# Optimization experiments

Measured on AMD Instinct MI355X. Metric: run time of the kernel, lower is better.

Reference implementation:

```python
import jax, jax.numpy as jnp
import numpy as np

D_MODEL = 1024
HIDDEN = 2048
D_STATE = 16
KERN = 3
BATCH = 2
SEQ = 2048


def _layernorm(x, g, b, eps=1e-5):
    m = jnp.mean(x, axis=-1, keepdims=True)
    v = jnp.var(x, axis=-1, keepdims=True)
    return (x - m) * jax.lax.rsqrt(v + eps) * g + b


def setup_inputs() -> dict:
    key = jax.random.key(0)
    ks = jax.random.split(key, 10)
    w_scale = 0.02  # keep pre-activations in a sane range (mimics trained-net init)
    return {
        "x": jax.random.normal(ks[0], (BATCH, SEQ, D_MODEL), jnp.float32),
        "W_x": jax.random.normal(ks[1], (HIDDEN, D_MODEL), jnp.float32) * w_scale,
        "b_x": jnp.zeros((HIDDEN,), jnp.float32),
        "W_g": jax.random.normal(ks[2], (HIDDEN, D_MODEL), jnp.float32) * w_scale,
        "b_g": jnp.zeros((HIDDEN,), jnp.float32),
        "conv_w": jax.random.normal(ks[3], (HIDDEN, 1, KERN), jnp.float32) * 0.3,
        "conv_b": jnp.zeros((HIDDEN,), jnp.float32),
        "A_raw": jax.random.normal(ks[4], (HIDDEN, D_STATE), jnp.float32),
        "B_ssm": jax.random.normal(ks[5], (HIDDEN, D_STATE), jnp.float32),
        "C_ssm": jax.random.normal(ks[6], (HIDDEN, D_STATE), jnp.float32),
        "W_dt": jax.random.normal(ks[7], (HIDDEN, D_MODEL), jnp.float32) * w_scale,
        "b_dt": jnp.zeros((HIDDEN,), jnp.float32),
        "W_out": jax.random.normal(ks[8], (D_MODEL, HIDDEN), jnp.float32) * w_scale,
        "b_out": jnp.zeros((D_MODEL,), jnp.float32),
        "ln_g": jnp.ones((D_MODEL,), jnp.float32),
        "ln_b": jnp.zeros((D_MODEL,), jnp.float32),
    }


def reference(x, W_x, b_x, W_g, b_g, conv_w, conv_b, A_raw, B_ssm, C_ssm,
              W_dt, b_dt, W_out, b_out, ln_g, ln_b):
    # projections: u, gate
    u = jnp.einsum('bld,hd->blh', x, W_x) + b_x                    # [B,L,H]
    g = jax.nn.sigmoid(jnp.einsum('bld,hd->blh', x, W_g) + b_g)    # [B,L,H]
    # depthwise conv over time (padding = kernel//2, 'same' for odd kernel)
    pad = conv_w.shape[-1] // 2
    h = jax.lax.conv_general_dilated(
        jnp.transpose(u, (0, 2, 1)), conv_w,
        window_strides=(1,), padding=[(pad, pad)],
        feature_group_count=conv_w.shape[0],
        dimension_numbers=('NCH', 'OIH', 'NCH')) + conv_b[None, :, None]
    h = jnp.transpose(h, (0, 2, 1))                                # [B,L,H]
    u = u * g + h * (1.0 - g)
    # time-invariant dt per channel (mean over batch & time, clamped)
    dt = jax.nn.softplus(jnp.einsum('bld,hd->blh', x, W_dt) + b_dt).mean(axis=(0, 1))
    dt = jnp.clip(dt, 1e-3, 2.0)                                   # [H]
    # discretize
    A = -jax.nn.softplus(A_raw)                                    # [H,S]
    A_d = jnp.exp(A * dt[:, None])                                 # [H,S]
    B_d = (A_d - 1.0) / (A + 1e-6) * B_ssm                         # [H,S]
    # selective scan: state s[b,h,k] = A_d*s + B_d*u_t ; y = <s, C>
    Bsz, L, H = u.shape
    S = A_d.shape[1]

    def step(carry, u_t):                                          # u_t: [B,H]
        new = A_d[None] * carry + B_d[None] * u_t[:, :, None]      # [B,H,S]
        y_t = jnp.einsum('bhs,hs->bh', new, C_ssm)
        return new, y_t

    init = jnp.zeros((Bsz, H, S), dtype=u.dtype)
    _, ys = jax.lax.scan(step, init, jnp.transpose(u, (1, 0, 2)))  # ys: [L,B,H]
    y = jnp.transpose(ys, (1, 0, 2))                               # [B,L,H]
    out = jnp.einsum('blh,dh->bld', y, W_out) + b_out
    return _layernorm(x + out, ln_g, ln_b)
```

## Files before the change

### kernel.cpp

```cpp
#include <hip/hip_runtime.h>
#include <math.h>

#define D_MODEL 1024
#define HIDDEN  2048
#define D_STATE 16
#define BATCH   2
#define SEQ     2048
#define NTOK    (BATCH*SEQ)
#define CHUNK   64
#define NCHUNK  (SEQ/CHUNK)

typedef __attribute__((ext_vector_type(8))) short bf16x8;
typedef __attribute__((ext_vector_type(8))) unsigned short ushort8;
typedef __attribute__((ext_vector_type(4))) float f32x4;

#define GLOAD_LDS16(gptr, lptr) \
    __builtin_amdgcn_global_load_lds((const __attribute__((address_space(1))) void*)(gptr), \
                                     (__attribute__((address_space(3))) void*)(lptr), 16, 0, 0)

__device__ __forceinline__ float softplus_f(float x) {
    return fmaxf(x, 0.0f) + log1pf(expf(-fabsf(x)));
}
__device__ __forceinline__ float sigmoid_f(float x) {
    return 1.0f / (1.0f + expf(-x));
}
__device__ __forceinline__ ushort f2bf(float f) {
    unsigned u = __float_as_uint(f);
    unsigned r = (u + 0x7fffu + ((u >> 16) & 1u)) >> 16;
    return (ushort)r;
}
__device__ __forceinline__ float bf2f(ushort u) {
    return __uint_as_float(((unsigned)u) << 16);
}

__global__ __launch_bounds__(256) void cvt_all(
    const float* __restrict__ x, const float* __restrict__ Wx,
    const float* __restrict__ Wg, const float* __restrict__ Wdt,
    const float* __restrict__ Wout, ushort* __restrict__ arena)
{
    int i = blockIdx.x * 256 + threadIdx.x;
    const float* src; int base;
    if      (i < 1048576) { src = x;    base = 0; }
    else if (i < 1572864) { src = Wx;   base = 1048576; }
    else if (i < 2097152) { src = Wg;   base = 1572864; }
    else if (i < 2621440) { src = Wdt;  base = 2097152; }
    else                  { src = Wout; base = 2621440; }
    float4 v = reinterpret_cast<const float4*>(src)[i - base];
    ushort4 o = { f2bf(v.x), f2bf(v.y), f2bf(v.z), f2bf(v.w) };
    reinterpret_cast<ushort4*>(arena)[i] = o;
}

__device__ __forceinline__ void kloop_dbuf(
    const ushort* __restrict__ A, const ushort* __restrict__ B,
    int K, int m0, int n0, ushort* As, ushort* Bs,
    f32x4 (&acc)[4][4], int lane, int w, int wm, int wn)
{
    const int lr   = lane >> 2;
    const int kc   = (lane & 3) * 8;
    const int quad = lane >> 4;
    const int fr   = lane & 15;

    const int slab0 = w * 2;
    const int r0 = slab0 * 16 + lr;
    const int r1 = r0 + 16;
    const size_t ga0 = (size_t)(m0 + r0) * K + kc;
    const size_t ga1 = (size_t)(m0 + r1) * K + kc;
    const size_t gb0 = (size_t)(n0 + r0) * K + kc;
    const size_t gb1 = (size_t)(n0 + r1) * K + kc;

    GLOAD_LDS16(A + ga0, &As[slab0 * 512]);
    GLOAD_LDS16(A + ga1, &As[slab0 * 512 + 512]);
    GLOAD_LDS16(B + gb0, &Bs[slab0 * 512]);
    GLOAD_LDS16(B + gb1, &Bs[slab0 * 512 + 512]);

    int buf = 0;
    for (int k0 = 0; k0 < K; k0 += 32) {
        __syncthreads();
        if (k0 + 32 < K) {
            const int nb = (buf ^ 1) * 4096;
            GLOAD_LDS16(A + ga0 + k0 + 32, &As[nb + slab0 * 512]);
            GLOAD_LDS16(A + ga1 + k0 + 32, &As[nb + slab0 * 512 + 512]);
            GLOAD_LDS16(B + gb0 + k0 + 32, &Bs[nb + slab0 * 512]);
            GLOAD_LDS16(B + gb1 + k0 + 32, &Bs[nb + slab0 * 512 + 512]);
        }
        const ushort* as = &As[buf * 4096];
        const ushort* bs = &Bs[buf * 4096];
        bf16x8 af[4], bfv[4];
        #pragma unroll
        for (int t = 0; t < 4; t++) {
            af[t]  = *reinterpret_cast<const bf16x8*>(&as[(wm * 64 + t * 16 + fr) * 32 + quad * 8]);
            bfv[t] = *reinterpret_cast<const bf16x8*>(&bs[(wn * 64 + t * 16 + fr) * 32 + quad * 8]);
        }
        #pragma unroll
        for (int i = 0; i < 4; i++)
            #pragma unroll
            for (int j = 0; j < 4; j++)
                acc[i][j] = __builtin_amdgcn_mfma_f32_16x16x32_bf16(af[i], bfv[j], acc[i][j], 0, 0, 0);
        buf ^= 1;
    }
}

__global__ __launch_bounds__(256) void proj_gemm_fused(
    const ushort* __restrict__ xbf, const ushort* __restrict__ Wcat,
    const float* __restrict__ b_x, const float* __restrict__ b_g,
    const float* __restrict__ b_dt, ushort* __restrict__ u_out,
    ushort* __restrict__ g_out, float* __restrict__ dt_sum)
{
    __shared__ ushort S[16384];
    ushort* As = S;
    ushort* Bs = S + 8192;
    const int tid = threadIdx.x, lane = tid & 63, w = tid >> 6;
    const int wm = w & 1, wn = w >> 1;
    const int m0 = blockIdx.y * 128, n0 = blockIdx.x * 128;
    const int quad = lane >> 4, fr = lane & 15;

    f32x4 acc[4][4];
    #pragma unroll
    for (int i = 0; i < 4; i++)
        #pragma unroll
        for (int j = 0; j < 4; j++)
            acc[i][j] = (f32x4){0.f, 0.f, 0.f, 0.f};

    kloop_dbuf(xbf, Wcat, D_MODEL, m0, n0, As, Bs, acc, lane, w, wm, wn);

    const int region = n0 >> 11;
    const int ncb = n0 & 2047;

    if (region == 2) {
        #pragma unroll
        for (int j = 0; j < 4; j++) {
            int n = ncb + wn * 64 + j * 16 + fr;
            float bj = b_dt[n];
            float s = 0.f;
            #pragma unroll
            for (int i = 0; i < 4; i++)
                #pragma unroll
                for (int r = 0; r < 4; r++)
                    s += softplus_f(acc[i][j][r] + bj);
            s += __shfl_xor(s, 16);
            s += __shfl_xor(s, 32);
            if (lane < 16) atomicAdd(&dt_sum[n], s);
        }
    } else {
        const float* bias = region ? b_g : b_x;
        ushort* out = region ? g_out : u_out;
        __syncthreads();
        ushort* Cs = S;
        #pragma unroll
        for (int j = 0; j < 4; j++) {
            int col = wn * 64 + j * 16 + fr;
            float bj = bias[ncb + col];
            #pragma unroll
            for (int i = 0; i < 4; i++) {
                int row = wm * 64 + i * 16 + quad * 4;
                #pragma unroll
                for (int r = 0; r < 4; r++) {
                    float v = acc[i][j][r] + bj;
                    if (region) v = sigmoid_f(v);
                    Cs[(row + r) * 128 + col] = f2bf(v);
                }
            }
        }
        __syncthreads();
        #pragma unroll
        for (int k = 0; k < 8; k++) {
            int v = k * 256 + tid;
            int row = v >> 4, c = (v & 15) * 8;
            *reinterpret_cast<ushort8*>(&out[(size_t)(m0 + row) * HIDDEN + ncb + c]) =
                *reinterpret_cast<const ushort8*>(&Cs[v * 8]);
        }
    }
}

__global__ __launch_bounds__(256) void gemm_out(
    const ushort* __restrict__ ybf, const ushort* __restrict__ Wout,
    const float* __restrict__ b_out, const float* __restrict__ x,
    float* __restrict__ resid)
{
    __shared__ ushort S[16384];
    ushort* As = S;
    ushort* Bs = S + 8192;
    const int tid = threadIdx.x, lane = tid & 63, w = tid >> 6;
    const int wm = w & 1, wn = w >> 1;
    const int m0 = blockIdx.y * 128, n0 = blockIdx.x * 128;
    const int quad = lane >> 4, fr = lane & 15;

    f32x4 acc[4][4];
    #pragma unroll
    for (int i = 0; i < 4; i++)
        #pragma unroll
        for (int j = 0; j < 4; j++)
            acc[i][j] = (f32x4){0.f, 0.f, 0.f, 0.f};

    kloop_dbuf(ybf, Wout, HIDDEN, m0, n0, As, Bs, acc, lane, w, wm, wn);

    float* Sf = (float*)S;
    __syncthreads();
    #pragma unroll
    for (int phase = 0; phase < 2; phase++) {
        if (wm == phase) {
            #pragma unroll
            for (int j = 0; j < 4; j++) {
                int col = wn * 64 + j * 16 + fr;
                float bj = b_out[n0 + col];
                #pragma unroll
                for (int i = 0; i < 4; i++) {
                    int row = i * 16 + quad * 4;
                    #pragma unroll
                    for (int r = 0; r < 4; r++)
                        Sf[(row + r) * 128 + col] = acc[i][j][r] + bj;
                }
            }
        }
        __syncthreads();
        #pragma unroll
        for (int k = 0; k < 8; k++) {
            int v = k * 256 + tid;
            int row = v >> 5, c = (v & 31) * 4;
            size_t off = (size_t)(m0 + phase * 64 + row) * D_MODEL + n0 + c;
            float4 xa = *reinterpret_cast<const float4*>(&x[off]);
            float4 cv = *reinterpret_cast<const float4*>(&Sf[v * 4]);
            float4 o = { cv.x + xa.x, cv.y + xa.y, cv.z + xa.z, cv.w + xa.w };
            *reinterpret_cast<float4*>(&resid[off]) = o;
        }
        __syncthreads();
    }
}

__global__ __launch_bounds__(256) void dt_finalize(
    const float* __restrict__ dt_sum, const float* __restrict__ A_raw,
    const float* __restrict__ B_ssm, float* __restrict__ A_d,
    float* __restrict__ B_d, float* __restrict__ A_dL)
{
    int i = blockIdx.x * 256 + threadIdx.x;
    if (i >= HIDDEN * D_STATE) return;
    int h = i >> 4;
    float dt = dt_sum[h] * (1.0f / NTOK);
    dt = fminf(fmaxf(dt, 1e-3f), 2.0f);
    float Av = -softplus_f(A_raw[i]);
    float Ad = expf(Av * dt);
    float Bd = (Ad - 1.0f) / (Av + 1e-6f) * B_ssm[i];
    A_d[i] = Ad;
    B_d[i] = Bd;
    A_dL[i] = expf(Av * dt * CHUNK);
}

__global__ __launch_bounds__(256) void scan_pass1(
    const ushort* __restrict__ u_bf, const ushort* __restrict__ g_bf,
    const float* __restrict__ conv_w, const float* __restrict__ conv_b,
    const float* __restrict__ A_d, const float* __restrict__ B_d,
    const float* __restrict__ C_ssm,
    ushort* __restrict__ ypart, float* __restrict__ states)
{
    int idx = blockIdx.x * 256 + threadIdx.x;
    int h  = idx & (HIDDEN - 1);
    int bc = idx >> 11;
    int c  = bc & (NCHUNK - 1);
    int b  = bc >> 5;
    float Ad[D_STATE], Bd[D_STATE], Cv[D_STATE], st[D_STATE];
    const float4* a4 = reinterpret_cast<const float4*>(A_d  + h * D_STATE);
    const float4* b4 = reinterpret_cast<const float4*>(B_d  + h * D_STATE);
    const float4* c4 = reinterpret_cast<const float4*>(C_ssm + h * D_STATE);
    #pragma unroll
    for (int q = 0; q < 4; q++) {
        float4 av = a4[q], bv = b4[q], cv = c4[q];
        Ad[q*4+0]=av.x; Ad[q*4+1]=av.y; Ad[q*4+2]=av.z; Ad[q*4+3]=av.w;
        Bd[q*4+0]=bv.x; Bd[q*4+1]=bv.y; Bd[q*4+2]=bv.z; Bd[q*4+3]=bv.w;
        Cv[q*4+0]=cv.x; Cv[q*4+1]=cv.y; Cv[q*4+2]=cv.z; Cv[q*4+3]=cv.w;
    }
    #pragma unroll
    for (int s = 0; s < D_STATE; s++) st[s] = 0.f;

    float w0 = conv_w[h * 3 + 0], w1 = conv_w[h * 3 + 1];
    float w2 = conv_w[h * 3 + 2], cb = conv_b[h];
    const int tok0 = c * CHUNK;
    const size_t base = ((size_t)b * SEQ + tok0) * HIDDEN + h;
    float u_prev = (tok0 > 0) ? bf2f(u_bf[base - HIDDEN]) : 0.f;
    float u_cur  = bf2f(u_bf[base]);
    for (int l = 0; l < CHUNK; l++) {
        float u_next = (tok0 + l + 1 < SEQ) ? bf2f(u_bf[base + (size_t)(l + 1) * HIDDEN]) : 0.f;
        float gv = bf2f(g_bf[base + (size_t)l * HIDDEN]);
        float conv = u_prev * w0 + u_cur * w1 + u_next * w2 + cb;
        float uv = u_cur * gv + conv * (1.0f - gv);
        float yv = 0.f;
        #pragma unroll
        for (int s = 0; s < D_STATE; s++) {
            st[s] = fmaf(Ad[s], st[s], Bd[s] * uv);
            yv = fmaf(st[s], Cv[s], yv);
        }
        ypart[base + (size_t)l * HIDDEN] = f2bf(yv);
        u_prev = u_cur; u_cur = u_next;
    }
    float4* sp = reinterpret_cast<float4*>(states + ((size_t)bc * HIDDEN + h) * D_STATE);
    #pragma unroll
    for (int q = 0; q < 4; q++)
        sp[q] = (float4){st[q*4+0], st[q*4+1], st[q*4+2], st[q*4+3]};
}

__global__ __launch_bounds__(256) void scan_pass2(
    float* __restrict__ states, const float* __restrict__ A_dL)
{
    int idx = blockIdx.x * 256 + threadIdx.x;
    int s = idx & 15;
    int h = (idx >> 4) & (HIDDEN - 1);
    int b = idx >> 15;
    float aL = A_dL[h * D_STATE + s];
    float carry = 0.f;
    for (int c = 0; c < NCHUNK; c++) {
        size_t addr = (((size_t)(b * NCHUNK + c) * HIDDEN) + h) * D_STATE + s;
        float fin = states[addr];
        states[addr] = carry;
        carry = fmaf(aL, carry, fin);
    }
}

__global__ __launch_bounds__(256) void scan_pass3(
    const ushort* __restrict__ ypart, const float* __restrict__ states,
    const float* __restrict__ A_d, const float* __restrict__ C_ssm,
    ushort* __restrict__ ybf)
{
    int idx = blockIdx.x * 256 + threadIdx.x;
    int h  = idx & (HIDDEN - 1);
    int bc = idx >> 11;
    int c  = bc & (NCHUNK - 1);
    int b  = bc >> 5;
    float Ad[D_STATE], t[D_STATE];
    const float* sp = states + ((size_t)bc * HIDDEN + h) * D_STATE;
    #pragma unroll
    for (int s = 0; s < D_STATE; s++) {
        float a = A_d[h * D_STATE + s];
        Ad[s] = a;
        t[s] = C_ssm[h * D_STATE + s] * a * sp[s];
    }
    const size_t base = ((size_t)b * SEQ + (size_t)c * CHUNK) * HIDDEN + h;
    for (int l = 0; l < CHUNK; l++) {
        float corr = 0.f;
        #pragma unroll
        for (int s = 0; s < D_STATE; s++) {
            corr += t[s];
            t[s] *= Ad[s];
        }
        ybf[base + (size_t)l * HIDDEN] = f2bf(bf2f(ypart[base + (size_t)l * HIDDEN]) + corr);
    }
}

__global__ __launch_bounds__(256) void ln_kernel(
    const float* __restrict__ resid, const float* __restrict__ ln_g,
    const float* __restrict__ ln_b, float* __restrict__ out)
{
    int row = blockIdx.x;
    int tid = threadIdx.x;
    const float4 v = reinterpret_cast<const float4*>(resid + (size_t)row * D_MODEL)[tid];
    float s  = v.x + v.y + v.z + v.w;
    float ss = v.x * v.x + v.y * v.y + v.z * v.z + v.w * v.w;
    #pragma unroll
    for (int off = 32; off > 0; off >>= 1) {
        s  += __shfl_down(s, off);
        ss += __shfl_down(ss, off);
    }
    __shared__ float sbuf[4], ssbuf[4];
    int wid = tid >> 6, lane = tid & 63;
    if (lane == 0) { sbuf[wid] = s; ssbuf[wid] = ss; }
    __syncthreads();
    float tot  = sbuf[0] + sbuf[1] + sbuf[2] + sbuf[3];
    float tot2 = ssbuf[0] + ssbuf[1] + ssbuf[2] + ssbuf[3];
    float mean = tot * (1.0f / D_MODEL);
    float var  = tot2 * (1.0f / D_MODEL) - mean * mean;
    float rstd = rsqrtf(var + 1e-5f);
    const float4 gv = reinterpret_cast<const float4*>(ln_g)[tid];
    const float4 bv = reinterpret_cast<const float4*>(ln_b)[tid];
    float4 o;
    o.x = (v.x - mean) * rstd * gv.x + bv.x;
    o.y = (v.y - mean) * rstd * gv.y + bv.y;
    o.z = (v.z - mean) * rstd * gv.z + bv.z;
    o.w = (v.w - mean) * rstd * gv.w + bv.w;
    reinterpret_cast<float4*>(out + (size_t)row * D_MODEL)[tid] = o;
}

extern "C" void kernel_launch(void* const* d_in, const int* in_sizes, int n_in,
                              void* d_out, int out_size, void* d_ws, size_t ws_size,
                              hipStream_t stream) {
    const float* x      = (const float*)d_in[0];
    const float* W_x    = (const float*)d_in[1];
    const float* b_x    = (const float*)d_in[2];
    const float* W_g    = (const float*)d_in[3];
    const float* b_g    = (const float*)d_in[4];
    const float* conv_w = (const float*)d_in[5];
    const float* conv_b = (const float*)d_in[6];
    const float* A_raw  = (const float*)d_in[7];
    const float* B_ssm  = (const float*)d_in[8];
    const float* C_ssm  = (const float*)d_in[9];
    const float* W_dt   = (const float*)d_in[10];
    const float* b_dt   = (const float*)d_in[11];
    const float* W_out  = (const float*)d_in[12];
    const float* b_out  = (const float*)d_in[13];
    const float* ln_g   = (const float*)d_in[14];
    const float* ln_b   = (const float*)d_in[15];

    char* W = (char*)d_ws;
    ushort* arena   = (ushort*)(W);
    ushort* x_bf    = arena;
    ushort* Wcat    = arena + 4194304;
    ushort* Wout_bf = arena + 10485760;
    ushort* u_bf    = (ushort*)(W + (24ull << 20));
    ushort* g_bf    = (ushort*)(W + (40ull << 20));
    ushort* ypart   = (ushort*)(W + (56ull << 20));
    float*  resid   = (float*)(W + (40ull << 20));
    float*  states  = (float*)(W + (72ull << 20));
    float*  dt_sum  = (float*)(W + (80ull << 20));
    float*  A_d     = (float*)(W + (80ull << 20) + 65536);
    float*  B_d     = (float*)(W + (80ull << 20) + 65536 + 131072);
    float*  A_dL    = (float*)(W + (80ull << 20) + 65536 + 262144);
    ushort* y_bf    = u_bf;

    hipMemsetAsync(dt_sum, 0, HIDDEN * sizeof(float), stream);

    dim3 blk(256);
    cvt_all<<<12288, blk, 0, stream>>>(x, W_x, W_g, W_dt, W_out, arena);

    dim3 grid_proj(3 * HIDDEN / 128, NTOK / 128);
    proj_gemm_fused<<<grid_proj, blk, 0, stream>>>(x_bf, Wcat, b_x, b_g, b_dt,
                                                   u_bf, g_bf, dt_sum);
    dt_finalize<<<(HIDDEN * D_STATE) / 256, blk, 0, stream>>>(dt_sum, A_raw, B_ssm,
                                                              A_d, B_d, A_dL);
    scan_pass1<<<(BATCH * NCHUNK * HIDDEN) / 256, blk, 0, stream>>>(
        u_bf, g_bf, conv_w, conv_b, A_d, B_d, C_ssm, ypart, states);
    scan_pass2<<<(BATCH * HIDDEN * D_STATE) / 256, blk, 0, stream>>>(states, A_dL);
    scan_pass3<<<(BATCH * NCHUNK * HIDDEN) / 256, blk, 0, stream>>>(ypart, states, A_d,
                                                                    C_ssm, y_bf);
    dim3 grid_out(D_MODEL / 128, NTOK / 128);
    gemm_out<<<grid_out, blk, 0, stream>>>(y_bf, Wout_bf, b_out, x, resid);
    ln_kernel<<<NTOK, blk, 0, stream>>>(resid, ln_g, ln_b, (float*)d_out);
}
```

Measured before the change: 318.0 us.

## Fold dt discretization into scan kernels, retile output GEMM, swap grid order

Removes the dt_finalize kernel and its A_d/B_d/A_dL buffers; the scan passes now recompute the discretized A and B from dt_sum and A_raw inline. The output GEMM becomes 64x128 tiles on 128-thread blocks with its own inlined double-buffered k-loop, doubling the block count to give more parallelism. Both GEMM grids are transposed so that consecutive blocks walk along M, which changes weight reuse in L2. Scan inner loops split the reduction across several accumulators to shorten dependency chains, at the cost of redundant exp/softplus work per thread.

```diff
diff --git a/kernel.cpp b/kernel.cpp
--- a/kernel.cpp
+++ b/kernel.cpp
@@ -111,7 +111,7 @@
     ushort* Bs = S + 8192;
     const int tid = threadIdx.x, lane = tid & 63, w = tid >> 6;
     const int wm = w & 1, wn = w >> 1;
-    const int m0 = blockIdx.y * 128, n0 = blockIdx.x * 128;
+    const int m0 = blockIdx.x * 128, n0 = blockIdx.y * 128;
     const int quad = lane >> 4, fr = lane & 15;
 
     f32x4 acc[4][4];
@@ -172,18 +172,20 @@
     }
 }
 
-__global__ __launch_bounds__(256) void gemm_out(
+__global__ __launch_bounds__(128) void gemm_out(
     const ushort* __restrict__ ybf, const ushort* __restrict__ Wout,
     const float* __restrict__ b_out, const float* __restrict__ x,
     float* __restrict__ resid)
 {
     __shared__ ushort S[16384];
     ushort* As = S;
-    ushort* Bs = S + 8192;
+    ushort* Bs = S + 4096;
     const int tid = threadIdx.x, lane = tid & 63, w = tid >> 6;
-    const int wm = w & 1, wn = w >> 1;
-    const int m0 = blockIdx.y * 128, n0 = blockIdx.x * 128;
+    const int wn = w;
+    const int m0 = blockIdx.x * 64, n0 = blockIdx.y * 128;
     const int quad = lane >> 4, fr = lane & 15;
+    const int lr = lane >> 2, kc = (lane & 3) * 8;
+    const int K = HIDDEN;
 
     f32x4 acc[4][4];
     #pragma unroll
@@ -192,64 +194,79 @@
         for (int j = 0; j < 4; j++)
             acc[i][j] = (f32x4){0.f, 0.f, 0.f, 0.f};
 
-    kloop_dbuf(ybf, Wout, HIDDEN, m0, n0, As, Bs, acc, lane, w, wm, wn);
+    const int sa0 = w * 2, sa1 = w * 2 + 1;
+    size_t gaddrA0 = (size_t)(m0 + sa0 * 16 + lr) * K + kc;
+    size_t gaddrA1 = (size_t)(m0 + sa1 * 16 + lr) * K + kc;
+    size_t gaddrB[4];
+    #pragma unroll
+    for (int j = 0; j < 4; j++)
+        gaddrB[j] = (size_t)(n0 + (w * 4 + j) * 16 + lr) * K + kc;
+
+    GLOAD_LDS16(ybf + gaddrA0, &As[sa0 * 512]);
+    GLOAD_LDS16(ybf + gaddrA1, &As[sa1 * 512]);
+    #pragma unroll
+    for (int j = 0; j < 4; j++)
+        GLOAD_LDS16(Wout + gaddrB[j], &Bs[(w * 4 + j) * 512]);
+
+    int buf = 0;
+    for (int k0 = 0; k0 < K; k0 += 32) {
+        __syncthreads();
+        if (k0 + 32 < K) {
+            const int nbA = (buf ^ 1) * 2048, nbB = (buf ^ 1) * 4096;
+            GLOAD_LDS16(ybf + gaddrA0 + k0 + 32, &As[nbA + sa0 * 512]);
+            GLOAD_LDS16(ybf + gaddrA1 + k0 + 32, &As[nbA + sa1 * 512]);
+            #pragma unroll
+            for (int j = 0; j < 4; j++)
+                GLOAD_LDS16(Wout + gaddrB[j] + k0 + 32, &Bs[nbB + (w * 4 + j) * 512]);
+        }
+        const ushort* as = &As[buf * 2048];
+        const ushort* bs = &Bs[buf * 4096];
+        bf16x8 af[4], bfv[4];
+        #pragma unroll
+        for (int t = 0; t < 4; t++) {
+            af[t]  = *reinterpret_cast<const bf16x8*>(&as[(t * 16 + fr) * 32 + quad * 8]);
+            bfv[t] = *reinterpret_cast<const bf16x8*>(&bs[(wn * 64 + t * 16 + fr) * 32 + quad * 8]);
+        }
+        #pragma unroll
+        for (int i = 0; i < 4; i++)
+            #pragma unroll
+            for (int j = 0; j < 4; j++)
+                acc[i][j] = __builtin_amdgcn_mfma_f32_16x16x32_bf16(af[i], bfv[j], acc[i][j], 0, 0, 0);
+        buf ^= 1;
+    }
 
     float* Sf = (float*)S;
     __syncthreads();
     #pragma unroll
-    for (int phase = 0; phase < 2; phase++) {
-        if (wm == phase) {
-            #pragma unroll
-            for (int j = 0; j < 4; j++) {
-                int col = wn * 64 + j * 16 + fr;
-                float bj = b_out[n0 + col];
-                #pragma unroll
-                for (int i = 0; i < 4; i++) {
-                    int row = i * 16 + quad * 4;
-                    #pragma unroll
-                    for (int r = 0; r < 4; r++)
-                        Sf[(row + r) * 128 + col] = acc[i][j][r] + bj;
-                }
-            }
-        }
-        __syncthreads();
-        #pragma unroll
-        for (int k = 0; k < 8; k++) {
-            int v = k * 256 + tid;
-            int row = v >> 5, c = (v & 31) * 4;
-            size_t off = (size_t)(m0 + phase * 64 + row) * D_MODEL + n0 + c;
-            float4 xa = *reinterpret_cast<const float4*>(&x[off]);
-            float4 cv = *reinterpret_cast<const float4*>(&Sf[v * 4]);
-            float4 o = { cv.x + xa.x, cv.y + xa.y, cv.z + xa.z, cv.w + xa.w };
-            *reinterpret_cast<float4*>(&resid[off]) = o;
-        }
-        __syncthreads();
-    }
-}
-
-__global__ __launch_bounds__(256) void dt_finalize(
-    const float* __restrict__ dt_sum, const float* __restrict__ A_raw,
-    const float* __restrict__ B_ssm, float* __restrict__ A_d,
-    float* __restrict__ B_d, float* __restrict__ A_dL)
-{
-    int i = blockIdx.x * 256 + threadIdx.x;
-    if (i >= HIDDEN * D_STATE) return;
-    int h = i >> 4;
-    float dt = dt_sum[h] * (1.0f / NTOK);
-    dt = fminf(fmaxf(dt, 1e-3f), 2.0f);
-    float Av = -softplus_f(A_raw[i]);
-    float Ad = expf(Av * dt);
-    float Bd = (Ad - 1.0f) / (Av + 1e-6f) * B_ssm[i];
-    A_d[i] = Ad;
-    B_d[i] = Bd;
-    A_dL[i] = expf(Av * dt * CHUNK);
+    for (int j = 0; j < 4; j++) {
+        int col = wn * 64 + j * 16 + fr;
+        float bj = b_out[n0 + col];
+        #pragma unroll
+        for (int i = 0; i < 4; i++) {
+            int row = i * 16 + quad * 4;
+            #pragma unroll
+            for (int r = 0; r < 4; r++)
+                Sf[(row + r) * 128 + col] = acc[i][j][r] + bj;
+        }
+    }
+    __syncthreads();
+    #pragma unroll
+    for (int k = 0; k < 16; k++) {
+        int v = k * 128 + tid;
+        int row = v >> 5, c = (v & 31) * 4;
+        size_t off = (size_t)(m0 + row) * D_MODEL + n0 + c;
+        float4 xa = *reinterpret_cast<const float4*>(&x[off]);
+        float4 cv = *reinterpret_cast<const float4*>(&Sf[v * 4]);
+        float4 o = { cv.x + xa.x, cv.y + xa.y, cv.z + xa.z, cv.w + xa.w };
+        *reinterpret_cast<float4*>(&resid[off]) = o;
+    }
 }
 
 __global__ __launch_bounds__(256) void scan_pass1(
     const ushort* __restrict__ u_bf, const ushort* __restrict__ g_bf,
     const float* __restrict__ conv_w, const float* __restrict__ conv_b,
-    const float* __restrict__ A_d, const float* __restrict__ B_d,
-    const float* __restrict__ C_ssm,
+    const float* __restrict__ dt_sum, const float* __restrict__ A_raw,
+    const float* __restrict__ B_ssm, const float* __restrict__ C_ssm,
     ushort* __restrict__ ypart, float* __restrict__ states)
 {
     int idx = blockIdx.x * 256 + threadIdx.x;
@@ -257,19 +274,17 @@
     int bc = idx >> 11;
     int c  = bc & (NCHUNK - 1);
     int b  = bc >> 5;
+    float dt = fminf(fmaxf(dt_sum[h] * (1.0f / NTOK), 1e-3f), 2.0f);
     float Ad[D_STATE], Bd[D_STATE], Cv[D_STATE], st[D_STATE];
-    const float4* a4 = reinterpret_cast<const float4*>(A_d  + h * D_STATE);
-    const float4* b4 = reinterpret_cast<const float4*>(B_d  + h * D_STATE);
-    const float4* c4 = reinterpret_cast<const float4*>(C_ssm + h * D_STATE);
-    #pragma unroll
-    for (int q = 0; q < 4; q++) {
-        float4 av = a4[q], bv = b4[q], cv = c4[q];
-        Ad[q*4+0]=av.x; Ad[q*4+1]=av.y; Ad[q*4+2]=av.z; Ad[q*4+3]=av.w;
-        Bd[q*4+0]=bv.x; Bd[q*4+1]=bv.y; Bd[q*4+2]=bv.z; Bd[q*4+3]=bv.w;
-        Cv[q*4+0]=cv.x; Cv[q*4+1]=cv.y; Cv[q*4+2]=cv.z; Cv[q*4+3]=cv.w;
-    }
-    #pragma unroll
-    for (int s = 0; s < D_STATE; s++) st[s] = 0.f;
+    #pragma unroll
+    for (int s = 0; s < D_STATE; s++) {
+        float Av = -softplus_f(A_raw[h * D_STATE + s]);
+        float a = expf(Av * dt);
+        Ad[s] = a;
+        Bd[s] = (a - 1.0f) / (Av + 1e-6f) * B_ssm[h * D_STATE + s];
+        Cv[s] = C_ssm[h * D_STATE + s];
+        st[s] = 0.f;
+    }
 
     float w0 = conv_w[h * 3 + 0], w1 = conv_w[h * 3 + 1];
     float w2 = conv_w[h * 3 + 2], cb = conv_b[h];
@@ -282,13 +297,19 @@
         float gv = bf2f(g_bf[base + (size_t)l * HIDDEN]);
         float conv = u_prev * w0 + u_cur * w1 + u_next * w2 + cb;
         float uv = u_cur * gv + conv * (1.0f - gv);
-        float yv = 0.f;
-        #pragma unroll
-        for (int s = 0; s < D_STATE; s++) {
-            st[s] = fmaf(Ad[s], st[s], Bd[s] * uv);
-            yv = fmaf(st[s], Cv[s], yv);
-        }
-        ypart[base + (size_t)l * HIDDEN] = f2bf(yv);
+        float y0 = 0.f, y1 = 0.f, y2 = 0.f, y3 = 0.f;
+        #pragma unroll
+        for (int s = 0; s < D_STATE; s += 4) {
+            st[s+0] = fmaf(Ad[s+0], st[s+0], Bd[s+0] * uv);
+            st[s+1] = fmaf(Ad[s+1], st[s+1], Bd[s+1] * uv);
+            st[s+2] = fmaf(Ad[s+2], st[s+2], Bd[s+2] * uv);
+            st[s+3] = fmaf(Ad[s+3], st[s+3], Bd[s+3] * uv);
+            y0 = fmaf(st[s+0], Cv[s+0], y0);
+            y1 = fmaf(st[s+1], Cv[s+1], y1);
+            y2 = fmaf(st[s+2], Cv[s+2], y2);
+            y3 = fmaf(st[s+3], Cv[s+3], y3);
+        }
+        ypart[base + (size_t)l * HIDDEN] = f2bf((y0 + y1) + (y2 + y3));
         u_prev = u_cur; u_cur = u_next;
     }
     float4* sp = reinterpret_cast<float4*>(states + ((size_t)bc * HIDDEN + h) * D_STATE);
@@ -298,13 +319,16 @@
 }
 
 __global__ __launch_bounds__(256) void scan_pass2(
-    float* __restrict__ states, const float* __restrict__ A_dL)
+    float* __restrict__ states, const float* __restrict__ dt_sum,
+    const float* __restrict__ A_raw)
 {
     int idx = blockIdx.x * 256 + threadIdx.x;
     int s = idx & 15;
     int h = (idx >> 4) & (HIDDEN - 1);
     int b = idx >> 15;
-    float aL = A_dL[h * D_STATE + s];
+    float dt = fminf(fmaxf(dt_sum[h] * (1.0f / NTOK), 1e-3f), 2.0f);
+    float Av = -softplus_f(A_raw[h * D_STATE + s]);
+    float aL = expf(Av * dt * CHUNK);
     float carry = 0.f;
     for (int c = 0; c < NCHUNK; c++) {
         size_t addr = (((size_t)(b * NCHUNK + c) * HIDDEN) + h) * D_STATE + s;
@@ -316,31 +340,35 @@
 
 __global__ __launch_bounds__(256) void scan_pass3(
     const ushort* __restrict__ ypart, const float* __restrict__ states,
-    const float* __restrict__ A_d, const float* __restrict__ C_ssm,
-    ushort* __restrict__ ybf)
+    const float* __restrict__ dt_sum, const float* __restrict__ A_raw,
+    const float* __restrict__ C_ssm, ushort* __restrict__ ybf)
 {
     int idx = blockIdx.x * 256 + threadIdx.x;
     int h  = idx & (HIDDEN - 1);
     int bc = idx >> 11;
     int c  = bc & (NCHUNK - 1);
     int b  = bc >> 5;
+    float dt = fminf(fmaxf(dt_sum[h] * (1.0f / NTOK), 1e-3f), 2.0f);
     float Ad[D_STATE], t[D_STATE];
     const float* sp = states + ((size_t)bc * HIDDEN + h) * D_STATE;
     #pragma unroll
     for (int s = 0; s < D_STATE; s++) {
-        float a = A_d[h * D_STATE + s];
+        float Av = -softplus_f(A_raw[h * D_STATE + s]);
+        float a = expf(Av * dt);
         Ad[s] = a;
         t[s] = C_ssm[h * D_STATE + s] * a * sp[s];
     }
     const size_t base = ((size_t)b * SEQ + (size_t)c * CHUNK) * HIDDEN + h;
     for (int l = 0; l < CHUNK; l++) {
-        float corr = 0.f;
-        #pragma unroll
-        for (int s = 0; s < D_STATE; s++) {
-            corr += t[s];
+        float c0 = 0.f, c1 = 0.f;
+        #pragma unroll
+        for (int s = 0; s < D_STATE; s += 2) {
+            c0 += t[s];
+            c1 += t[s + 1];
             t[s] *= Ad[s];
-        }
-        ybf[base + (size_t)l * HIDDEN] = f2bf(bf2f(ypart[base + (size_t)l * HIDDEN]) + corr);
+            t[s + 1] *= Ad[s + 1];
+        }
+        ybf[base + (size_t)l * HIDDEN] = f2bf(bf2f(ypart[base + (size_t)l * HIDDEN]) + (c0 + c1));
     }
 }
 
@@ -408,9 +436,6 @@
     float*  resid   = (float*)(W + (40ull << 20));
     float*  states  = (float*)(W + (72ull << 20));
     float*  dt_sum  = (float*)(W + (80ull << 20));
-    float*  A_d     = (float*)(W + (80ull << 20) + 65536);
-    float*  B_d     = (float*)(W + (80ull << 20) + 65536 + 131072);
-    float*  A_dL    = (float*)(W + (80ull << 20) + 65536 + 262144);
     ushort* y_bf    = u_bf;
 
     hipMemsetAsync(dt_sum, 0, HIDDEN * sizeof(float), stream);
@@ -418,17 +443,15 @@
     dim3 blk(256);
     cvt_all<<<12288, blk, 0, stream>>>(x, W_x, W_g, W_dt, W_out, arena);
 
-    dim3 grid_proj(3 * HIDDEN / 128, NTOK / 128);
+    dim3 grid_proj(NTOK / 128, 3 * HIDDEN / 128);
     proj_gemm_fused<<<grid_proj, blk, 0, stream>>>(x_bf, Wcat, b_x, b_g, b_dt,
                                                    u_bf, g_bf, dt_sum);
-    dt_finalize<<<(HIDDEN * D_STATE) / 256, blk, 0, stream>>>(dt_sum, A_raw, B_ssm,
-                                                              A_d, B_d, A_dL);
     scan_pass1<<<(BATCH * NCHUNK * HIDDEN) / 256, blk, 0, stream>>>(
-        u_bf, g_bf, conv_w, conv_b, A_d, B_d, C_ssm, ypart, states);
-    scan_pass2<<<(BATCH * HIDDEN * D_STATE) / 256, blk, 0, stream>>>(states, A_dL);
-    scan_pass3<<<(BATCH * NCHUNK * HIDDEN) / 256, blk, 0, stream>>>(ypart, states, A_d,
-                                                                    C_ssm, y_bf);
-    dim3 grid_out(D_MODEL / 128, NTOK / 128);
-    gemm_out<<<grid_out, blk, 0, stream>>>(y_bf, Wout_bf, b_out, x, resid);
+        u_bf, g_bf, conv_w, conv_b, dt_sum, A_raw, B_ssm, C_ssm, ypart, states);
+    scan_pass2<<<(BATCH * HIDDEN * D_STATE) / 256, blk, 0, stream>>>(states, dt_sum, A_raw);
+    scan_pass3<<<(BATCH * NCHUNK * HIDDEN) / 256, blk, 0, stream>>>(ypart, states, dt_sum,
+                                                                    A_raw, C_ssm, y_bf);
+    dim3 grid_out(NTOK / 64, D_MODEL / 128);
+    gemm_out<<<grid_out, dim3(128), 0, stream>>>(y_bf, Wout_bf, b_out, x, resid);
     ln_kernel<<<NTOK, blk, 0, stream>>>(resid, ln_g, ln_b, (float*)d_out);
 }
```

After: 323.2 us. Within noise of the previous version (+1.6%).

## Triple-buffer GEMM k-loop with explicit waitcnt, swap grid order, split scan FMA chains

Applied to the files above, without the earlier changes.

Replaces the double-buffered LDS k-loop in both GEMMs with a three-stage pipeline. Loads are issued two iterations ahead and synchronised with explicit s_waitcnt vmcnt(4) and s_barrier, which hides more global latency at the cost of extra LDS. The launch grid is transposed so consecutive blocks walk the M dimension, which changes L2 reuse of the weight tiles. The scan pass1 and pass3 reductions are split into several independent accumulators to shorten dependent FMA and add chains.

```diff
diff --git a/kernel.cpp b/kernel.cpp
--- a/kernel.cpp
+++ b/kernel.cpp
@@ -50,7 +50,7 @@
     reinterpret_cast<ushort4*>(arena)[i] = o;
 }
 
-__device__ __forceinline__ void kloop_dbuf(
+__device__ __forceinline__ void kloop_pipe3(
     const ushort* __restrict__ A, const ushort* __restrict__ B,
     int K, int m0, int n0, ushort* As, ushort* Bs,
     f32x4 (&acc)[4][4], int lane, int w, int wm, int wn)
@@ -68,21 +68,27 @@
     const size_t gb0 = (size_t)(n0 + r0) * K + kc;
     const size_t gb1 = (size_t)(n0 + r1) * K + kc;
 
-    GLOAD_LDS16(A + ga0, &As[slab0 * 512]);
-    GLOAD_LDS16(A + ga1, &As[slab0 * 512 + 512]);
-    GLOAD_LDS16(B + gb0, &Bs[slab0 * 512]);
-    GLOAD_LDS16(B + gb1, &Bs[slab0 * 512 + 512]);
+    const int niter = K / 32;
+    GLOAD_LDS16(A + ga0,      &As[slab0 * 512]);
+    GLOAD_LDS16(A + ga1,      &As[slab0 * 512 + 512]);
+    GLOAD_LDS16(B + gb0,      &Bs[slab0 * 512]);
+    GLOAD_LDS16(B + gb1,      &Bs[slab0 * 512 + 512]);
+    GLOAD_LDS16(A + ga0 + 32, &As[4096 + slab0 * 512]);
+    GLOAD_LDS16(A + ga1 + 32, &As[4096 + slab0 * 512 + 512]);
+    GLOAD_LDS16(B + gb0 + 32, &Bs[4096 + slab0 * 512]);
+    GLOAD_LDS16(B + gb1 + 32, &Bs[4096 + slab0 * 512 + 512]);
 
     int buf = 0;
-    for (int k0 = 0; k0 < K; k0 += 32) {
-        __syncthreads();
-        if (k0 + 32 < K) {
-            const int nb = (buf ^ 1) * 4096;
-            GLOAD_LDS16(A + ga0 + k0 + 32, &As[nb + slab0 * 512]);
-            GLOAD_LDS16(A + ga1 + k0 + 32, &As[nb + slab0 * 512 + 512]);
-            GLOAD_LDS16(B + gb0 + k0 + 32, &Bs[nb + slab0 * 512]);
-            GLOAD_LDS16(B + gb1 + k0 + 32, &Bs[nb + slab0 * 512 + 512]);
-        }
+    for (int i = 0; i < niter; i++) {
+        asm volatile("s_waitcnt vmcnt(4) lgkmcnt(0)" ::: "memory");
+        asm volatile("s_barrier" ::: "memory");
+        int nb = buf + 2; if (nb >= 3) nb -= 3;
+        const size_t koff = (i + 2 < niter) ? (size_t)(i + 2) * 32 : 0;
+        GLOAD_LDS16(A + ga0 + koff, &As[nb * 4096 + slab0 * 512]);
+        GLOAD_LDS16(A + ga1 + koff, &As[nb * 4096 + slab0 * 512 + 512]);
+        GLOAD_LDS16(B + gb0 + koff, &Bs[nb * 4096 + slab0 * 512]);
+        GLOAD_LDS16(B + gb1 + koff, &Bs[nb * 4096 + slab0 * 512 + 512]);
+
         const ushort* as = &As[buf * 4096];
         const ushort* bs = &Bs[buf * 4096];
         bf16x8 af[4], bfv[4];
@@ -92,12 +98,14 @@
             bfv[t] = *reinterpret_cast<const bf16x8*>(&bs[(wn * 64 + t * 16 + fr) * 32 + quad * 8]);
         }
         #pragma unroll
-        for (int i = 0; i < 4; i++)
+        for (int ii = 0; ii < 4; ii++)
             #pragma unroll
-            for (int j = 0; j < 4; j++)
-                acc[i][j] = __builtin_amdgcn_mfma_f32_16x16x32_bf16(af[i], bfv[j], acc[i][j], 0, 0, 0);
-        buf ^= 1;
-    }
+            for (int jj = 0; jj < 4; jj++)
+                acc[ii][jj] = __builtin_amdgcn_mfma_f32_16x16x32_bf16(af[ii], bfv[jj], acc[ii][jj], 0, 0, 0);
+        buf = (buf == 2) ? 0 : buf + 1;
+    }
+    asm volatile("s_waitcnt vmcnt(0) lgkmcnt(0)" ::: "memory");
+    asm volatile("s_barrier" ::: "memory");
 }
 
 __global__ __launch_bounds__(256) void proj_gemm_fused(
@@ -106,12 +114,12 @@
     const float* __restrict__ b_dt, ushort* __restrict__ u_out,
     ushort* __restrict__ g_out, float* __restrict__ dt_sum)
 {
-    __shared__ ushort S[16384];
+    __shared__ ushort S[24576];
     ushort* As = S;
-    ushort* Bs = S + 8192;
+    ushort* Bs = S + 12288;
     const int tid = threadIdx.x, lane = tid & 63, w = tid >> 6;
     const int wm = w & 1, wn = w >> 1;
-    const int m0 = blockIdx.y * 128, n0 = blockIdx.x * 128;
+    const int m0 = blockIdx.x * 128, n0 = blockIdx.y * 128;
     const int quad = lane >> 4, fr = lane & 15;
 
     f32x4 acc[4][4];
@@ -121,7 +129,7 @@
         for (int j = 0; j < 4; j++)
             acc[i][j] = (f32x4){0.f, 0.f, 0.f, 0.f};
 
-    kloop_dbuf(xbf, Wcat, D_MODEL, m0, n0, As, Bs, acc, lane, w, wm, wn);
+    kloop_pipe3(xbf, Wcat, D_MODEL, m0, n0, As, Bs, acc, lane, w, wm, wn);
 
     const int region = n0 >> 11;
     const int ncb = n0 & 2047;
@@ -144,7 +152,6 @@
     } else {
         const float* bias = region ? b_g : b_x;
         ushort* out = region ? g_out : u_out;
-        __syncthreads();
         ushort* Cs = S;
         #pragma unroll
         for (int j = 0; j < 4; j++) {
@@ -177,12 +184,12 @@
     const float* __restrict__ b_out, const float* __restrict__ x,
     float* __restrict__ resid)
 {
-    __shared__ ushort S[16384];
+    __shared__ ushort S[24576];
     ushort* As = S;
-    ushort* Bs = S + 8192;
+    ushort* Bs = S + 12288;
     const int tid = threadIdx.x, lane = tid & 63, w = tid >> 6;
     const int wm = w & 1, wn = w >> 1;
-    const int m0 = blockIdx.y * 128, n0 = blockIdx.x * 128;
+    const int m0 = blockIdx.x * 128, n0 = blockIdx.y * 128;
     const int quad = lane >> 4, fr = lane & 15;
 
     f32x4 acc[4][4];
@@ -192,10 +199,9 @@
         for (int j = 0; j < 4; j++)
             acc[i][j] = (f32x4){0.f, 0.f, 0.f, 0.f};
 
-    kloop_dbuf(ybf, Wout, HIDDEN, m0, n0, As, Bs, acc, lane, w, wm, wn);
+    kloop_pipe3(ybf, Wout, HIDDEN, m0, n0, As, Bs, acc, lane, w, wm, wn);
 
     float* Sf = (float*)S;
-    __syncthreads();
     #pragma unroll
     for (int phase = 0; phase < 2; phase++) {
         if (wm == phase) {
@@ -282,13 +288,19 @@
         float gv = bf2f(g_bf[base + (size_t)l * HIDDEN]);
         float conv = u_prev * w0 + u_cur * w1 + u_next * w2 + cb;
         float uv = u_cur * gv + conv * (1.0f - gv);
-        float yv = 0.f;
-        #pragma unroll
-        for (int s = 0; s < D_STATE; s++) {
-            st[s] = fmaf(Ad[s], st[s], Bd[s] * uv);
-            yv = fmaf(st[s], Cv[s], yv);
-        }
-        ypart[base + (size_t)l * HIDDEN] = f2bf(yv);
+        float y0 = 0.f, y1 = 0.f, y2 = 0.f, y3 = 0.f;
+        #pragma unroll
+        for (int s = 0; s < D_STATE; s += 4) {
+            st[s+0] = fmaf(Ad[s+0], st[s+0], Bd[s+0] * uv);
+            st[s+1] = fmaf(Ad[s+1], st[s+1], Bd[s+1] * uv);
+            st[s+2] = fmaf(Ad[s+2], st[s+2], Bd[s+2] * uv);
+            st[s+3] = fmaf(Ad[s+3], st[s+3], Bd[s+3] * uv);
+            y0 = fmaf(st[s+0], Cv[s+0], y0);
+            y1 = fmaf(st[s+1], Cv[s+1], y1);
+            y2 = fmaf(st[s+2], Cv[s+2], y2);
+            y3 = fmaf(st[s+3], Cv[s+3], y3);
+        }
+        ypart[base + (size_t)l * HIDDEN] = f2bf((y0 + y1) + (y2 + y3));
         u_prev = u_cur; u_cur = u_next;
     }
     float4* sp = reinterpret_cast<float4*>(states + ((size_t)bc * HIDDEN + h) * D_STATE);
@@ -334,13 +346,15 @@
     }
     const size_t base = ((size_t)b * SEQ + (size_t)c * CHUNK) * HIDDEN + h;
     for (int l = 0; l < CHUNK; l++) {
-        float corr = 0.f;
-        #pragma unroll
-        for (int s = 0; s < D_STATE; s++) {
-            corr += t[s];
+        float c0 = 0.f, c1 = 0.f;
+        #pragma unroll
+        for (int s = 0; s < D_STATE; s += 2) {
+            c0 += t[s];
+            c1 += t[s + 1];
             t[s] *= Ad[s];
-        }
-        ybf[base + (size_t)l * HIDDEN] = f2bf(bf2f(ypart[base + (size_t)l * HIDDEN]) + corr);
+            t[s + 1] *= Ad[s + 1];
+        }
+        ybf[base + (size_t)l * HIDDEN] = f2bf(bf2f(ypart[base + (size_t)l * HIDDEN]) + (c0 + c1));
     }
 }
 
@@ -418,7 +432,7 @@
     dim3 blk(256);
     cvt_all<<<12288, blk, 0, stream>>>(x, W_x, W_g, W_dt, W_out, arena);
 
-    dim3 grid_proj(3 * HIDDEN / 128, NTOK / 128);
+    dim3 grid_proj(NTOK / 128, 3 * HIDDEN / 128);
     proj_gemm_fused<<<grid_proj, blk, 0, stream>>>(x_bf, Wcat, b_x, b_g, b_dt,
                                                    u_bf, g_bf, dt_sum);
     dt_finalize<<<(HIDDEN * D_STATE) / 256, blk, 0, stream>>>(dt_sum, A_raw, B_ssm,
@@ -428,7 +442,7 @@
     scan_pass2<<<(BATCH * HIDDEN * D_STATE) / 256, blk, 0, stream>>>(states, A_dL);
     scan_pass3<<<(BATCH * NCHUNK * HIDDEN) / 256, blk, 0, stream>>>(ypart, states, A_d,
                                                                     C_ssm, y_bf);
-    dim3 grid_out(D_MODEL / 128, NTOK / 128);
+    dim3 grid_out(NTOK / 128, D_MODEL / 128);
     gemm_out<<<grid_out, blk, 0, stream>>>(y_bf, Wout_bf, b_out, x, resid);
     ln_kernel<<<NTOK, blk, 0, stream>>>(resid, ln_g, ln_b, (float*)d_out);
 }
```

Result: faster. 295.6 us (-7.0%).
